# Performance work log

Hardware: AMD Instinct MI355X
Metric: run time of the kernel (lower is better)

Reference implementation:

```python
import jax, jax.numpy as jnp
import numpy as np

N = 200000      # nodes
C = 256         # scalar channels
VC = 16         # vector channels
VD = 3          # vector spatial dim
M = 50000       # number of motifs (segments)


def setup_inputs() -> dict:
    key = jax.random.key(0)
    ks, kv, kb, kw1, kb1, kw2, kb2 = jax.random.split(key, 7)
    s = jax.random.normal(ks, (N, C), dtype=jnp.float32)
    v = jax.random.normal(kv, (N, VC, VD), dtype=jnp.float32)
    motif_batch = jax.random.randint(kb, (N,), 0, M, dtype=jnp.int64)
    # Linear(channels, channels)
    Ws = jax.random.normal(kw1, (C, C), dtype=jnp.float32) / np.sqrt(C)
    bs = jax.random.normal(kb1, (C,), dtype=jnp.float32) * 0.01
    # Linear(16, 16)
    Wv = jax.random.normal(kw2, (VC, VC), dtype=jnp.float32) / np.sqrt(VC)
    bv = jax.random.normal(kb2, (VC,), dtype=jnp.float32) * 0.01
    return {"s": s, "v": v, "motif_batch": motif_batch,
            "Ws": Ws, "bs": bs, "Wv": Wv, "bv": bv}


def _scatter_mean(x, seg, num_segments):
    # robust scatter mean: sum / max(count, 1)
    sums = jax.ops.segment_sum(x, seg, num_segments=num_segments)
    cnt = jax.ops.segment_sum(jnp.ones((x.shape[0],), x.dtype), seg,
                              num_segments=num_segments)
    cnt = jnp.maximum(cnt, 1.0)
    return sums / cnt.reshape((num_segments,) + (1,) * (x.ndim - 1))


def reference(s, v, motif_batch, Ws, bs, Wv, bv):
    seg = motif_batch.reshape(-1)
    s_motif = _scatter_mean(s, seg, M)            # [M, C]
    v_motif = _scatter_mean(v, seg, M)            # [M, VC, VD]
    s_out = s_motif @ Ws.T + bs                   # [M, C]
    # v_pool(v_motif.transpose(1,2)).transpose(1,2):
    # Linear over the VC axis, spatial dim untouched
    v_out = jnp.einsum('mcd,oc->mod', v_motif, Wv) + bv[None, :, None]
    return (s_out, v_out)
```

## Files before the change

### kernel.cpp

```cpp
#include <hip/hip_runtime.h>

#define N_NODES 200000
#define C 256
#define VC 16
#define VD 3
#define VDIM (VC * VD)
#define M_MOTIFS 50000
#define CAP 64

#define TM 64
#define NODE_BLOCKS ((N_NODES + 255) / 256)
#define CVT_BLOCKS  ((C * C) / (256 * 4))
#define FUSED_BLOCKS ((M_MOTIFS + TM - 1) / TM)

typedef __attribute__((ext_vector_type(8))) __bf16 bf16x8;
typedef __attribute__((ext_vector_type(4))) float f32x4;

__device__ __forceinline__ unsigned short f2bf(float x) {
  unsigned u = __builtin_bit_cast(unsigned, x);
  u += 0x7fffu + ((u >> 16) & 1u);
  return (unsigned short)(u >> 16);
}

__global__ __launch_bounds__(256) void fill_kernel(
    const int* __restrict__ seg, int* __restrict__ cnt,
    int* __restrict__ nodelist, const float* __restrict__ Ws,
    unsigned short* __restrict__ Wsb) {
  int b = blockIdx.x, t = threadIdx.x;
  if (b < NODE_BLOCKS) {
    int i = b * 256 + t;
    if (i < N_NODES) {
      int m = seg[i];
      int r = atomicAdd(&cnt[m], 1);
      if (r < CAP) nodelist[(size_t)m * CAP + r] = i;
    }
  } else {
    int i = ((b - NODE_BLOCKS) * 256 + t) * 4;
    float4 w = *(const float4*)(Ws + i);
    ushort4 o;
    o.x = f2bf(w.x); o.y = f2bf(w.y); o.z = f2bf(w.z); o.w = f2bf(w.w);
    *(ushort4*)(Wsb + i) = o;
  }
}

__global__ __launch_bounds__(256, 3) void fused_kernel(
    const float* __restrict__ s, const float* __restrict__ v,
    const int* __restrict__ cnt, const int* __restrict__ nodelist,
    const unsigned short* __restrict__ Wsb, const float* __restrict__ bs,
    const float* __restrict__ Wv, const float* __restrict__ bv,
    float* __restrict__ s_out, float* __restrict__ v_out) {
  __shared__ unsigned short As[TM * C];

  int tid = threadIdx.x;
  int wave = tid >> 6, lane = tid & 63;
  int bm0 = blockIdx.x * TM;
  int m0w = bm0 + wave * 16;

  int kv = 0;
  if (lane < 16) {
    int mm = m0w + lane;
    if (mm < M_MOTIFS) kv = cnt[mm];
  }
  int rA = lane >> 3, sl = lane & 7;
  int kA = __shfl(kv, rA, 64);
  int kB = __shfl(kv, 8 + rA, 64);
  int id8a = 0, id8b = 0;
  if (sl < kA) id8a = nodelist[(size_t)(m0w + rA) * CAP + sl];
  if (sl < kB) id8b = nodelist[(size_t)(m0w + 8 + rA) * CAP + sl];

  for (int r = 0; r < 16; ++r) {
    int m = m0w + r;
    int k = __shfl(kv, r, 64);
    int idr = (r < 8) ? id8a : id8b;
    int rb = (r & 7) * 8;
    float4 acc = make_float4(0.f, 0.f, 0.f, 0.f);
    float vacc = 0.f;
    int kc = min(k, CAP);
    int n8 = min(kc, 8);
    int jj = 0;
    for (; jj + 4 <= n8; jj += 4) {
      int i0 = __shfl(idr, rb + jj + 0, 64);
      int i1 = __shfl(idr, rb + jj + 1, 64);
      int i2 = __shfl(idr, rb + jj + 2, 64);
      int i3 = __shfl(idr, rb + jj + 3, 64);
      float4 a = ((const float4*)(s + (size_t)i0 * C))[lane];
      float4 b = ((const float4*)(s + (size_t)i1 * C))[lane];
      float4 c = ((const float4*)(s + (size_t)i2 * C))[lane];
      float4 d = ((const float4*)(s + (size_t)i3 * C))[lane];
      acc.x += (a.x + b.x) + (c.x + d.x);
      acc.y += (a.y + b.y) + (c.y + d.y);
      acc.z += (a.z + b.z) + (c.z + d.z);
      acc.w += (a.w + b.w) + (c.w + d.w);
      if (lane < VDIM) {
        float va = v[(size_t)i0 * VDIM + lane];
        float vb = v[(size_t)i1 * VDIM + lane];
        float vc = v[(size_t)i2 * VDIM + lane];
        float vd = v[(size_t)i3 * VDIM + lane];
        vacc += (va + vb) + (vc + vd);
      }
    }
    for (; jj < n8; ++jj) {
      int i0 = __shfl(idr, rb + jj, 64);
      float4 a = ((const float4*)(s + (size_t)i0 * C))[lane];
      acc.x += a.x; acc.y += a.y; acc.z += a.z; acc.w += a.w;
      if (lane < VDIM) vacc += v[(size_t)i0 * VDIM + lane];
    }
    if (kc > 8) {
      int nid2 = 0;
      if (lane >= 8 && lane < kc) nid2 = nodelist[(size_t)m * CAP + lane];
      for (int j = 8; j < kc; ++j) {
        int i0 = __shfl(nid2, j, 64);
        float4 a = ((const float4*)(s + (size_t)i0 * C))[lane];
        acc.x += a.x; acc.y += a.y; acc.z += a.z; acc.w += a.w;
        if (lane < VDIM) vacc += v[(size_t)i0 * VDIM + lane];
      }
    }

    float rc = 1.0f / (float)max(k, 1);
    ushort4 o;
    o.x = f2bf(acc.x * rc); o.y = f2bf(acc.y * rc);
    o.z = f2bf(acc.z * rc); o.w = f2bf(acc.w * rc);
    int rblk = wave * 16 + r;
    *(ushort4*)&As[rblk * C + ((lane * 4) ^ ((rblk & 7) << 3))] = o;

    float vm = vacc * rc;
    if (lane < VDIM && m < M_MOTIFS) {
      int oo = lane / 3, d = lane - oo * 3;
      float vo = bv[oo];
#pragma unroll
      for (int c = 0; c < VC; ++c)
        vo += Wv[oo * VC + c] * __shfl(vm, c * 3 + d, 64);
      v_out[(size_t)m * VDIM + lane] = vo;
    }
  }

  __syncthreads();

  int rl = lane & 15, kq = (lane >> 4) * 8;
  int wn0 = wave * 64;
  int xorv = (rl & 7) << 3;
  f32x4 acc4[4][4] = {};
  for (int k0 = 0; k0 < C; k0 += 32) {
    bf16x8 af[4], bfr[4];
#pragma unroll
    for (int i = 0; i < 4; ++i)
      af[i] = *(const bf16x8*)&As[(i * 16 + rl) * C + ((k0 + kq) ^ xorv)];
#pragma unroll
    for (int j = 0; j < 4; ++j)
      bfr[j] = *(const bf16x8*)(Wsb + (size_t)(wn0 + j * 16 + rl) * C + k0 + kq);
#pragma unroll
    for (int i = 0; i < 4; ++i)
#pragma unroll
      for (int j = 0; j < 4; ++j)
        acc4[i][j] = __builtin_amdgcn_mfma_f32_16x16x32_bf16(
            af[i], bfr[j], acc4[i][j], 0, 0, 0);
  }

  int rq = (lane >> 4) * 4;
#pragma unroll
  for (int j = 0; j < 4; ++j) {
    int cn = wn0 + j * 16 + rl;
    float bias = bs[cn];
#pragma unroll
    for (int i = 0; i < 4; ++i) {
#pragma unroll
      for (int rr = 0; rr < 4; ++rr) {
        int gm = bm0 + i * 16 + rq + rr;
        if (gm < M_MOTIFS) s_out[(size_t)gm * C + cn] = acc4[i][j][rr] + bias;
      }
    }
  }
}

extern "C" void kernel_launch(void* const* d_in, const int* in_sizes, int n_in,
                              void* d_out, int out_size, void* d_ws, size_t ws_size,
                              hipStream_t stream) {
  const float* s  = (const float*)d_in[0];
  const float* v  = (const float*)d_in[1];
  const int*   seg = (const int*)d_in[2];
  const float* Ws = (const float*)d_in[3];
  const float* bs = (const float*)d_in[4];
  const float* Wv = (const float*)d_in[5];
  const float* bv = (const float*)d_in[6];

  float* out   = (float*)d_out;
  float* s_out = out;
  float* v_out = out + (size_t)M_MOTIFS * C;

  int* cnt      = (int*)d_ws;
  int* nodelist = cnt + M_MOTIFS;
  unsigned short* Wsb = (unsigned short*)(nodelist + (size_t)M_MOTIFS * CAP);

  hipMemsetAsync(cnt, 0, M_MOTIFS * sizeof(int), stream);
  fill_kernel<<<NODE_BLOCKS + CVT_BLOCKS, 256, 0, stream>>>(seg, cnt, nodelist,
                                                            Ws, Wsb);
  fused_kernel<<<FUSED_BLOCKS, 256, 0, stream>>>(s, v, cnt, nodelist, Wsb, bs,
                                                 Wv, bv, s_out, v_out);
}
```

Baseline: 109.8 us.

## Shrink motif tile to 16 rows per block to raise occupancy and parallelism

Reduces the per-block motif tile from 64 to 16 rows, so each wave gathers 4 motifs instead of 16. The grid grows fourfold and the launch-bounds occupancy hint doubles. Node ids are prefetched 16 per motif with one load per lane, and the MFMA stage shrinks to one A fragment per wave. Smaller blocks should spread gather latency across more waves, but each block now reloads the whole bf16 weight matrix for fewer rows, and segments beyond 16 nodes read their ids with per-iteration scalar loads. Bounds checks are dropped on the assumption that M divides evenly by 16. The shared tile is still declared as TM*C, so it shrinks with TM.

```diff
diff --git a/kernel.cpp b/kernel.cpp
--- a/kernel.cpp
+++ b/kernel.cpp
@@ -8,10 +8,10 @@
 #define M_MOTIFS 50000
 #define CAP 64
 
-#define TM 64
+#define TM 16
 #define NODE_BLOCKS ((N_NODES + 255) / 256)
 #define CVT_BLOCKS  ((C * C) / (256 * 4))
-#define FUSED_BLOCKS ((M_MOTIFS + TM - 1) / TM)
+#define FUSED_BLOCKS (M_MOTIFS / TM)
 
 typedef __attribute__((ext_vector_type(8))) __bf16 bf16x8;
 typedef __attribute__((ext_vector_type(4))) float f32x4;
@@ -43,7 +43,7 @@
   }
 }
 
-__global__ __launch_bounds__(256, 3) void fused_kernel(
+__global__ __launch_bounds__(256, 6) void fused_kernel(
     const float* __restrict__ s, const float* __restrict__ v,
     const int* __restrict__ cnt, const int* __restrict__ nodelist,
     const unsigned short* __restrict__ Wsb, const float* __restrict__ bs,
@@ -54,35 +54,27 @@
   int tid = threadIdx.x;
   int wave = tid >> 6, lane = tid & 63;
   int bm0 = blockIdx.x * TM;
-  int m0w = bm0 + wave * 16;
+  int m0w = bm0 + wave * 4;
 
-  int kv = 0;
-  if (lane < 16) {
-    int mm = m0w + lane;
-    if (mm < M_MOTIFS) kv = cnt[mm];
-  }
-  int rA = lane >> 3, sl = lane & 7;
-  int kA = __shfl(kv, rA, 64);
-  int kB = __shfl(kv, 8 + rA, 64);
-  int id8a = 0, id8b = 0;
-  if (sl < kA) id8a = nodelist[(size_t)(m0w + rA) * CAP + sl];
-  if (sl < kB) id8b = nodelist[(size_t)(m0w + 8 + rA) * CAP + sl];
+  int kvv = 0;
+  if (lane < 4) kvv = cnt[m0w + lane];
+  int mr = lane >> 4, sl = lane & 15;
+  int idv = nodelist[(size_t)(m0w + mr) * CAP + sl];
 
-  for (int r = 0; r < 16; ++r) {
+  for (int r = 0; r < 4; ++r) {
     int m = m0w + r;
-    int k = __shfl(kv, r, 64);
-    int idr = (r < 8) ? id8a : id8b;
-    int rb = (r & 7) * 8;
+    int k = __shfl(kvv, r, 64);
+    int kc = min(k, CAP);
+    int n16 = min(kc, 16);
+    int rb = r * 16;
     float4 acc = make_float4(0.f, 0.f, 0.f, 0.f);
     float vacc = 0.f;
-    int kc = min(k, CAP);
-    int n8 = min(kc, 8);
     int jj = 0;
-    for (; jj + 4 <= n8; jj += 4) {
-      int i0 = __shfl(idr, rb + jj + 0, 64);
-      int i1 = __shfl(idr, rb + jj + 1, 64);
-      int i2 = __shfl(idr, rb + jj + 2, 64);
-      int i3 = __shfl(idr, rb + jj + 3, 64);
+    for (; jj + 4 <= n16; jj += 4) {
+      int i0 = __shfl(idv, rb + jj + 0, 64);
+      int i1 = __shfl(idv, rb + jj + 1, 64);
+      int i2 = __shfl(idv, rb + jj + 2, 64);
+      int i3 = __shfl(idv, rb + jj + 3, 64);
       float4 a = ((const float4*)(s + (size_t)i0 * C))[lane];
       float4 b = ((const float4*)(s + (size_t)i1 * C))[lane];
       float4 c = ((const float4*)(s + (size_t)i2 * C))[lane];
@@ -99,37 +91,33 @@
         vacc += (va + vb) + (vc + vd);
       }
     }
-    for (; jj < n8; ++jj) {
-      int i0 = __shfl(idr, rb + jj, 64);
+    for (; jj < n16; ++jj) {
+      int i0 = __shfl(idv, rb + jj, 64);
       float4 a = ((const float4*)(s + (size_t)i0 * C))[lane];
       acc.x += a.x; acc.y += a.y; acc.z += a.z; acc.w += a.w;
       if (lane < VDIM) vacc += v[(size_t)i0 * VDIM + lane];
     }
-    if (kc > 8) {
-      int nid2 = 0;
-      if (lane >= 8 && lane < kc) nid2 = nodelist[(size_t)m * CAP + lane];
-      for (int j = 8; j < kc; ++j) {
-        int i0 = __shfl(nid2, j, 64);
-        float4 a = ((const float4*)(s + (size_t)i0 * C))[lane];
-        acc.x += a.x; acc.y += a.y; acc.z += a.z; acc.w += a.w;
-        if (lane < VDIM) vacc += v[(size_t)i0 * VDIM + lane];
-      }
+    for (int j = 16; j < kc; ++j) {
+      int i0 = nodelist[(size_t)m * CAP + j];
+      float4 a = ((const float4*)(s + (size_t)i0 * C))[lane];
+      acc.x += a.x; acc.y += a.y; acc.z += a.z; acc.w += a.w;
+      if (lane < VDIM) vacc += v[(size_t)i0 * VDIM + lane];
     }
 
     float rc = 1.0f / (float)max(k, 1);
     ushort4 o;
     o.x = f2bf(acc.x * rc); o.y = f2bf(acc.y * rc);
     o.z = f2bf(acc.z * rc); o.w = f2bf(acc.w * rc);
-    int rblk = wave * 16 + r;
+    int rblk = (wave << 2) + r;
     *(ushort4*)&As[rblk * C + ((lane * 4) ^ ((rblk & 7) << 3))] = o;
 
     float vm = vacc * rc;
-    if (lane < VDIM && m < M_MOTIFS) {
+    if (lane < VDIM) {
       int oo = lane / 3, d = lane - oo * 3;
       float vo = bv[oo];
 #pragma unroll
-      for (int c = 0; c < VC; ++c)
-        vo += Wv[oo * VC + c] * __shfl(vm, c * 3 + d, 64);
+      for (int c2 = 0; c2 < VC; ++c2)
+        vo += Wv[oo * VC + c2] * __shfl(vm, c2 * 3 + d, 64);
       v_out[(size_t)m * VDIM + lane] = vo;
     }
   }
@@ -139,21 +127,18 @@
   int rl = lane & 15, kq = (lane >> 4) * 8;
   int wn0 = wave * 64;
   int xorv = (rl & 7) << 3;
-  f32x4 acc4[4][4] = {};
+  f32x4 acc4[4] = {};
+#pragma unroll
   for (int k0 = 0; k0 < C; k0 += 32) {
-    bf16x8 af[4], bfr[4];
-#pragma unroll
-    for (int i = 0; i < 4; ++i)
-      af[i] = *(const bf16x8*)&As[(i * 16 + rl) * C + ((k0 + kq) ^ xorv)];
+    bf16x8 af = *(const bf16x8*)&As[rl * C + ((k0 + kq) ^ xorv)];
+    bf16x8 bfr[4];
 #pragma unroll
     for (int j = 0; j < 4; ++j)
       bfr[j] = *(const bf16x8*)(Wsb + (size_t)(wn0 + j * 16 + rl) * C + k0 + kq);
 #pragma unroll
-    for (int i = 0; i < 4; ++i)
-#pragma unroll
-      for (int j = 0; j < 4; ++j)
-        acc4[i][j] = __builtin_amdgcn_mfma_f32_16x16x32_bf16(
-            af[i], bfr[j], acc4[i][j], 0, 0, 0);
+    for (int j = 0; j < 4; ++j)
+      acc4[j] = __builtin_amdgcn_mfma_f32_16x16x32_bf16(af, bfr[j], acc4[j],
+                                                        0, 0, 0);
   }
 
   int rq = (lane >> 4) * 4;
@@ -162,12 +147,9 @@
     int cn = wn0 + j * 16 + rl;
     float bias = bs[cn];
 #pragma unroll
-    for (int i = 0; i < 4; ++i) {
-#pragma unroll
-      for (int rr = 0; rr < 4; ++rr) {
-        int gm = bm0 + i * 16 + rq + rr;
-        if (gm < M_MOTIFS) s_out[(size_t)gm * C + cn] = acc4[i][j][rr] + bias;
-      }
+    for (int rr = 0; rr < 4; ++rr) {
+      int gm = bm0 + rq + rr;
+      s_out[(size_t)gm * C + cn] = acc4[j][rr] + bias;
     }
   }
 }
```

Result: slower. 120.7 us (+9.9%).
